# Performance work log

Measured on AMD Instinct MI355X. Metric: run time of the kernel, lower is better.

The kernel has to match this reference:

```python
import jax, jax.numpy as jnp
import numpy as np

N = 100000   # nodes
E = 3200000  # edges
F = 128      # num_features
H = 20       # hidden dim (hard-coded in source)
C = 10       # num_classes
EPS = 1e-5


def setup_inputs() -> dict:
    key = jax.random.key(0)
    ks = jax.random.split(key, 16)
    x = jax.random.normal(ks[0], (N, F), jnp.float32)
    edge_index = jax.random.randint(ks[1], (2, E), 0, N)
    edge_weights = jnp.ones((E,), jnp.float32)

    def lin_init(k, fan_in, shape):
        s = 1.0 / np.sqrt(fan_in)
        return jax.random.uniform(k, shape, jnp.float32, -s, s)

    return {
        "x": x,
        "edge_index": edge_index,
        "edge_weights": edge_weights,
        "W1": lin_init(ks[2], F, (F, H)), "b1": jnp.zeros((H,), jnp.float32),
        "g1": jnp.ones((H,), jnp.float32), "be1": jnp.zeros((H,), jnp.float32),
        "W2": lin_init(ks[3], H, (H, H)), "b2": jnp.zeros((H,), jnp.float32),
        "g2": jnp.ones((H,), jnp.float32), "be2": jnp.zeros((H,), jnp.float32),
        "W3": lin_init(ks[4], H, (H, H)), "b3": jnp.zeros((H,), jnp.float32),
        "Wl": lin_init(ks[5], 3 * H, (3 * H, C)), "bl": lin_init(ks[6], 3 * H, (C,)),
    }


def gcn_conv(x, src, dst, ew, W, b, n):
    # PyG GCNConv: transform, add self-loops, symmetric deg^-1/2 normalization, scatter-add.
    h = x @ W  # [N, out]
    loop = jnp.arange(n)
    src2 = jnp.concatenate([src, loop])
    dst2 = jnp.concatenate([dst, loop])
    ew2 = jnp.concatenate([ew, jnp.ones((n,), x.dtype)])
    deg = jax.ops.segment_sum(ew2, dst2, num_segments=n)
    dinv = jnp.where(deg > 0, jax.lax.rsqrt(deg), 0.0)
    coef = (dinv[src2] * ew2 * dinv[dst2])[:, None]  # [E+N, 1]
    out = jax.ops.segment_sum(h[src2] * coef, dst2, num_segments=n)
    return out + b


def batch_norm(x, g, b):
    m = x.mean(axis=0)
    v = x.var(axis=0)
    return (x - m) * jax.lax.rsqrt(v + EPS) * g + b


def reference(x, edge_index, edge_weights, W1, b1, g1, be1, W2, b2, g2, be2, W3, b3, Wl, bl):
    src, dst = edge_index[0], edge_index[1]
    n = x.shape[0]
    o1 = batch_norm(jax.nn.relu(gcn_conv(x, src, dst, edge_weights, W1, b1, n)), g1, be1)
    o2 = batch_norm(jax.nn.relu(gcn_conv(o1, src, dst, edge_weights, W2, b2, n)), g2, be2)
    o3 = jax.nn.relu(gcn_conv(o2, src, dst, edge_weights, W3, b3, n))
    emb = jnp.concatenate([o1, o2, o3], axis=1)  # [N, 60]
    return emb @ Wl + bl
```

## Files before the change

kernel.cpp:

```cpp
#include <hip/hip_runtime.h>
#include <hip/hip_fp16.h>


#define HD 20
#define HSS 32
#define EPS 1e-5f
#define BSH 7
#define NBMAX 1024
#define CAP 5632
#define CAPE 2816

typedef float __attribute__((ext_vector_type(4))) f4v;

__device__ __forceinline__ float4 ntld4(const float* p) {
    f4v v = __builtin_nontemporal_load((const f4v*)p);
    return make_float4(v.x, v.y, v.z, v.w);
}

__global__ __launch_bounds__(1024)
void init_kernel(int* bcnt, float* stats, float* zero20, int nbv) {
    int t = threadIdx.x;
    if (t < nbv) bcnt[t] = 0;
    if (t < 80) stats[t] = 0.0f;
    if (t < HD) zero20[t] = 0.0f;
}

__global__ __launch_bounds__(256)
void bucket_hist_kernel(const int* __restrict__ dst, int* __restrict__ bcnt,
                        int E, int chunk, int nbv) {
    __shared__ int lh[NBMAX];
    for (int i = threadIdx.x; i < nbv; i += 256) lh[i] = 0;
    __syncthreads();
    int s = blockIdx.x * chunk;
    int e = s + chunk; if (e > E) e = E;
    for (int j = s + threadIdx.x; j < e; j += 256)
        atomicAdd(&lh[dst[j] >> BSH], 1);
    __syncthreads();
    for (int i = threadIdx.x; i < nbv; i += 256)
        if (lh[i]) atomicAdd(&bcnt[i], lh[i]);
}

__global__ __launch_bounds__(1024)
void bucket_scan_kernel(const int* __restrict__ bcnt, int* __restrict__ bstart,
                        int* __restrict__ bcur, int* __restrict__ row_start,
                        int n, int E, int nbv) {
    __shared__ int s[1024];
    int t = threadIdx.x;
    int v = (t < nbv) ? bcnt[t] : 0;
    s[t] = v;
    __syncthreads();
    for (int off = 1; off < 1024; off <<= 1) {
        int u = (t >= off) ? s[t - off] : 0;
        __syncthreads();
        s[t] += u;
        __syncthreads();
    }
    if (t < nbv) { int st = s[t] - v; bstart[t] = st; bcur[t] = st; }
    if (t == 0) { bstart[nbv] = E; row_start[n] = E; }
}

__global__ __launch_bounds__(256)
void scatter_kernel(const int* __restrict__ src, const int* __restrict__ dst,
                    const float* __restrict__ ew, int* __restrict__ bcur,
                    int2* __restrict__ tmp, int E, int chunk, int nbv) {
    __shared__ int lh[NBMAX];
    __shared__ int lbase[NBMAX];
    for (int i = threadIdx.x; i < nbv; i += 256) lh[i] = 0;
    __syncthreads();
    int s = blockIdx.x * chunk;
    int e = s + chunk; if (e > E) e = E;
    for (int j = s + threadIdx.x; j < e; j += 256)
        atomicAdd(&lh[dst[j] >> BSH], 1);
    __syncthreads();
    for (int i = threadIdx.x; i < nbv; i += 256) {
        int c = lh[i];
        lbase[i] = c ? atomicAdd(&bcur[i], c) : 0;
        lh[i] = 0;
    }
    __syncthreads();
    for (int j = s + threadIdx.x; j < e; j += 256) {
        int d = dst[j];
        int b = d >> BSH;
        int pos = atomicAdd(&lh[b], 1);
        tmp[lbase[b] + pos] = make_int2(src[j] | ((d & ((1 << BSH) - 1)) << 20),
                                        __float_as_int(ew[j]));
    }
}

__global__ __launch_bounds__(256)
void finalize_kernel(const int2* __restrict__ tmp, const int* __restrict__ bstart,
                     int2* __restrict__ se, int* __restrict__ row_start,
                     float* __restrict__ dinv, int n) {
    __shared__ int hist[128];
    __shared__ float degs[128];
    __shared__ int off[128];
    __shared__ int cur[128];
    __shared__ int2 stage[CAP];
    int b = blockIdx.x;
    int s0 = bstart[b], s1 = bstart[b + 1];
    int cnt = s1 - s0;
    int t = threadIdx.x;
    if (t < 128) { hist[t] = 0; degs[t] = 0.0f; cur[t] = 0; }
    __syncthreads();
    for (int j = s0 + t; j < s1; j += 256) {
        int2 r = tmp[j];
        int l = r.x >> 20;
        atomicAdd(&hist[l], 1);
        atomicAdd(&degs[l], __int_as_float(r.y));
    }
    __syncthreads();
    if (t < 128) off[t] = hist[t];
    __syncthreads();
    for (int o = 1; o < 128; o <<= 1) {
        int u = (t < 128 && t >= o) ? off[t - o] : 0;
        __syncthreads();
        if (t < 128) off[t] += u;
        __syncthreads();
    }
    if (t < 128) {
        int node = (b << BSH) + t;
        if (node < n) {
            row_start[node] = s0 + off[t] - hist[t];
            dinv[node] = rsqrtf(1.0f + degs[t]);
        }
    }
    __syncthreads();
    if (cnt <= CAP) {
        for (int j = s0 + t; j < s1; j += 256) {
            int2 r = tmp[j];
            int l = r.x >> 20;
            int p = (off[l] - hist[l]) + atomicAdd(&cur[l], 1);
            stage[p] = make_int2(r.x & 0xFFFFF, r.y);
        }
        __syncthreads();
        for (int k = t; k < cnt; k += 256) se[s0 + k] = stage[k];
    } else {
        for (int j = s0 + t; j < s1; j += 256) {
            int2 r = tmp[j];
            int l = r.x >> 20;
            int p = (off[l] - hist[l]) + atomicAdd(&cur[l], 1);
            se[s0 + p] = make_int2(r.x & 0xFFFFF, r.y);
        }
    }
}

template<int FIN, int NPB>
__global__ __launch_bounds__(256)
void gemm_kernel(const float* __restrict__ in, const float* __restrict__ W,
                 const float* __restrict__ cvec, const float* __restrict__ dinv,
                 __half* __restrict__ hs, int n) {
    __shared__ float sWt[HD][FIN + 4];
    __shared__ float sIn[NPB][FIN + 4];
    __shared__ float sC[HD];
    for (int i = threadIdx.x; i < FIN * HD; i += 256) {
        int k = i / HD, f = i % HD;
        sWt[f][k] = W[i];
    }
    if (threadIdx.x < HD) sC[threadIdx.x] = cvec[threadIdx.x];
    int base = blockIdx.x * NPB;
    int nb = n - base; if (nb > NPB) nb = NPB;
    int lim = n * FIN;
    const int Q = FIN / 4;
    for (int i = threadIdx.x; i < NPB * Q; i += 256) {
        int row = i / Q, c = (i % Q) * 4;
        int g = (base + row) * FIN + c;
        *(float4*)&sIn[row][c] = (g < lim) ? ntld4(&in[g])
                                           : make_float4(0.f, 0.f, 0.f, 0.f);
    }
    __syncthreads();
    for (int idx = threadIdx.x; idx < NPB * HD; idx += 256) {
        int nl = idx / HD, f = idx % HD;
        float4 a = make_float4(0.f, 0.f, 0.f, 0.f);
        #pragma unroll 4
        for (int k = 0; k < FIN; k += 4) {
            float4 x4 = *(const float4*)&sIn[nl][k];
            float4 w4 = *(const float4*)&sWt[f][k];
            a.x = fmaf(x4.x, w4.x, a.x);
            a.y = fmaf(x4.y, w4.y, a.y);
            a.z = fmaf(x4.z, w4.z, a.z);
            a.w = fmaf(x4.w, w4.w, a.w);
        }
        if (nl < nb)
            hs[(size_t)(base + nl) * HSS + f] = __float2half_rn(
                (((a.x + a.y) + (a.z + a.w)) + sC[f]) * dinv[base + nl]);
    }
}

#define FMA4(A, V, W) \
    A.x = fmaf(V.x, W, A.x); A.y = fmaf(V.y, W, A.y); \
    A.z = fmaf(V.z, W, A.z); A.w = fmaf(V.w, W, A.w);

__device__ __forceinline__ float4 h4f2(uint2 u) {
    float2 f0 = __half22float2(*reinterpret_cast<const __half2*>(&u.x));
    float2 f1 = __half22float2(*reinterpret_cast<const __half2*>(&u.y));
    return make_float4(f0.x, f0.y, f1.x, f1.y);
}

#define ROWLD(Q0, Q1, Q2, SRC) { \
    const uint4* pa_ = (const uint4*)(hsb + (size_t)(SRC) * HSS); \
    Q0 = pa_[0]; Q1 = pa_[1]; \
    Q2 = *(const uint2*)(pa_ + 2); }

#define AGG_LOOP(EDGEAT)                                                     \
    {                                                                        \
        int2 e = EDGEAT(j);                                                  \
        float w = __int_as_float(e.y);                                       \
        uint4 c0, c1; uint2 c2; ROWLD(c0, c1, c2, e.x)                       \
        while (true) {                                                       \
            int jn = j + 4;                                                  \
            bool more = jn < s1;                                             \
            int jp = more ? jn : j;             \
            int2 en = EDGEAT(jp);                                            \
            uint4 n0, n1; uint2 n2; ROWLD(n0, n1, n2, en.x)                  \
            float wn = __int_as_float(en.y);                                 \
            float4 v0 = h4f2(make_uint2(c0.x, c0.y));                        \
            float4 v1 = h4f2(make_uint2(c0.z, c0.w));                        \
            float4 v2 = h4f2(make_uint2(c1.x, c1.y));                        \
            float4 v3 = h4f2(make_uint2(c1.z, c1.w));                        \
            float4 v4 = h4f2(c2);                                            \
            FMA4(a0, v0, w) FMA4(a1, v1, w) FMA4(a2, v2, w)                  \
            FMA4(a3, v3, w) FMA4(a4, v4, w)                                  \
            if (!more) break;                                                \
            j = jn; w = wn;                                                  \
            c0 = n0; c1 = n1; c2 = n2;                                       \
        }                                                                    \
    }

#define EDGE_LDS(jj) sse[(jj) - sb0]
#define EDGE_GBL(jj) se[(jj)]

template<int MODE>
__global__ __launch_bounds__(256)
void agg_kernel(const __half* __restrict__ hsb, const float* __restrict__ dinv,
                const int* __restrict__ row_start, const int2* __restrict__ se,
                const float* __restrict__ bias, float* __restrict__ out,
                float* __restrict__ stat_sum, float* __restrict__ stat_sq,
                const float* __restrict__ o1, const float* __restrict__ o2,
                const float* __restrict__ Wlp, const float* __restrict__ blp,
                int n) {
    __shared__ int2 sse[CAPE];
    __shared__ float ls[HD], lq[HD];
    __shared__ float sW[600];
    __shared__ float sb[10];
    int base = blockIdx.x * 64;
    int nEnd = base + 64; if (nEnd > n) nEnd = n;
    int sb0 = row_start[base];
    int sb1 = row_start[nEnd];
    int span = sb1 - sb0;
    bool ok = (span <= CAPE);
    if (MODE == 0) {
        if (threadIdx.x < HD) { ls[threadIdx.x] = 0.0f; lq[threadIdx.x] = 0.0f; }
    } else {
        for (int i = threadIdx.x; i < 600; i += 256) sW[i] = Wlp[i];
        if (threadIdx.x < 10) sb[threadIdx.x] = blp[threadIdx.x];
    }
    if (ok) {
        for (int k = threadIdx.x; k < span; k += 256) {
            long long v = __builtin_nontemporal_load(
                (const long long*)(se + sb0 + k));
            sse[k] = *(const int2*)&v;
        }
    }
    __syncthreads();
    int i = base + (threadIdx.x >> 2), lane = threadIdx.x & 3;
    if (i < n) {
        float di = dinv[i];
        int s0 = row_start[i], s1 = row_start[i + 1];
        float4 a0, a1, a2, a3, a4;
        if (lane == 0) {
            uint4 y0, y1; uint2 y2;
            ROWLD(y0, y1, y2, i)
            a0 = h4f2(make_uint2(y0.x, y0.y));
            a1 = h4f2(make_uint2(y0.z, y0.w));
            a2 = h4f2(make_uint2(y1.x, y1.y));
            a3 = h4f2(make_uint2(y1.z, y1.w));
            a4 = h4f2(y2);
        } else {
            a0 = a1 = a2 = a3 = a4 = make_float4(0.f, 0.f, 0.f, 0.f);
        }
        int j = s0 + lane;
        if (j < s1) {
            if (ok) { AGG_LOOP(EDGE_LDS) }
            else    { AGG_LOOP(EDGE_GBL) }
        }
        #define REDX(A, M) \
            A.x += __shfl_xor(A.x, M); A.y += __shfl_xor(A.y, M); \
            A.z += __shfl_xor(A.z, M); A.w += __shfl_xor(A.w, M);
        #define RED4L(A) REDX(A, 1) REDX(A, 2)
        RED4L(a0) RED4L(a1) RED4L(a2) RED4L(a3) RED4L(a4)
        float4 acc[5] = {a0, a1, a2, a3, a4};
        float va[HD];
        #pragma unroll
        for (int q = 0; q < 5; ++q) {
            float4 bb = *(const float4*)(bias + 4 * q);
            va[4 * q + 0] = fmaxf(fmaf(acc[q].x, di, bb.x), 0.0f);
            va[4 * q + 1] = fmaxf(fmaf(acc[q].y, di, bb.y), 0.0f);
            va[4 * q + 2] = fmaxf(fmaf(acc[q].z, di, bb.z), 0.0f);
            va[4 * q + 3] = fmaxf(fmaf(acc[q].w, di, bb.w), 0.0f);
        }
        if (MODE == 0) {
            if (lane == 0) {
                #pragma unroll
                for (int q = 0; q < 5; ++q) {
                    ((float4*)out)[i * 5 + q] = make_float4(
                        va[4 * q], va[4 * q + 1], va[4 * q + 2], va[4 * q + 3]);
                    int f = 4 * q;
                    atomicAdd(&ls[f + 0], va[f + 0]); atomicAdd(&lq[f + 0], va[f + 0] * va[f + 0]);
                    atomicAdd(&ls[f + 1], va[f + 1]); atomicAdd(&lq[f + 1], va[f + 1] * va[f + 1]);
                    atomicAdd(&ls[f + 2], va[f + 2]); atomicAdd(&lq[f + 2], va[f + 2] * va[f + 2]);
                    atomicAdd(&ls[f + 3], va[f + 3]); atomicAdd(&lq[f + 3], va[f + 3] * va[f + 3]);
                }
            }
        } else {
            float r1[HD], r2[HD];
            #pragma unroll
            for (int q = 0; q < 5; ++q) {
                *(float4*)&r1[4 * q] = ((const float4*)(o1 + (size_t)i * HD))[q];
                *(float4*)&r2[4 * q] = ((const float4*)(o2 + (size_t)i * HD))[q];
            }
            for (int c = lane; c < 10; c += 4) {
                float s = sb[c];
                #pragma unroll
                for (int k = 0; k < HD; ++k) s = fmaf(r1[k], sW[k * 10 + c], s);
                #pragma unroll
                for (int k = 0; k < HD; ++k) s = fmaf(r2[k], sW[(HD + k) * 10 + c], s);
                #pragma unroll
                for (int k = 0; k < HD; ++k) s = fmaf(va[k], sW[(2 * HD + k) * 10 + c], s);
                out[(size_t)i * 10 + c] = s;
            }
        }
    }
    if (MODE == 0) {
        __syncthreads();
        if (threadIdx.x < HD) {
            atomicAdd(&stat_sum[threadIdx.x], ls[threadIdx.x]);
            atomicAdd(&stat_sq[threadIdx.x], lq[threadIdx.x]);
        }
    }
}

__global__ __launch_bounds__(512)
void bn_adjust_kernel(const float* __restrict__ sum, const float* __restrict__ sq,
                      const float* __restrict__ g, const float* __restrict__ be,
                      const float* __restrict__ W, float* __restrict__ scsh_out,
                      float* __restrict__ Wp, float* __restrict__ cvec, int n) {
    __shared__ float ssc[HD], ssh[HD];
    int t = threadIdx.x;
    if (t < HD) {
        float inv_n = 1.0f / (float)n;
        float m = sum[t] * inv_n;
        float var = sq[t] * inv_n - m * m;
        float sc = g[t] * rsqrtf(var + EPS);
        float sh = be[t] - m * sc;
        ssc[t] = sc; ssh[t] = sh;
        scsh_out[t] = sc; scsh_out[HD + t] = sh;
    }
    __syncthreads();
    if (t < HD * HD) Wp[t] = ssc[t / HD] * W[t];
    if (t < HD) {
        float acc = 0.0f;
        #pragma unroll
        for (int k = 0; k < HD; ++k) acc = fmaf(ssh[k], W[k * HD + t], acc);
        cvec[t] = acc;
    }
}

__global__ __launch_bounds__(640)
void bn_adjust2_kernel(const float* __restrict__ sum, const float* __restrict__ sq,
                       const float* __restrict__ g, const float* __restrict__ be,
                       const float* __restrict__ W, float* __restrict__ scsh_out,
                       float* __restrict__ Wp, float* __restrict__ cvec,
                       const float* __restrict__ Wl, const float* __restrict__ bl,
                       const float* __restrict__ scsh1,
                       float* __restrict__ Wlp, float* __restrict__ blp, int n) {
    __shared__ float ssc[HD], ssh[HD];
    int t = threadIdx.x;
    if (t < HD) {
        float inv_n = 1.0f / (float)n;
        float m = sum[t] * inv_n;
        float var = sq[t] * inv_n - m * m;
        float sc = g[t] * rsqrtf(var + EPS);
        float sh = be[t] - m * sc;
        ssc[t] = sc; ssh[t] = sh;
        scsh_out[t] = sc; scsh_out[HD + t] = sh;
    }
    __syncthreads();
    if (t < HD * HD) Wp[t] = ssc[t / HD] * W[t];
    if (t < HD) {
        float acc = 0.0f;
        #pragma unroll
        for (int k = 0; k < HD; ++k) acc = fmaf(ssh[k], W[k * HD + t], acc);
        cvec[t] = acc;
    }
    if (t < 600) {
        int k = t / 10;
        float s = (k < HD) ? scsh1[k] : (k < 2 * HD) ? ssc[k - HD] : 1.0f;
        Wlp[t] = s * Wl[t];
    }
    if (t < 10) {
        float acc = bl[t];
        #pragma unroll
        for (int k = 0; k < HD; ++k) acc = fmaf(scsh1[HD + k], Wl[k * 10 + t], acc);
        #pragma unroll
        for (int k = 0; k < HD; ++k) acc = fmaf(ssh[k], Wl[(HD + k) * 10 + t], acc);
        blp[t] = acc;
    }
}

extern "C" void kernel_launch(void* const* d_in, const int* in_sizes, int n_in,
                              void* d_out, int out_size, void* d_ws, size_t ws_size,
                              hipStream_t stream) {
    const float* x   = (const float*)d_in[0];
    const int*   ei  = (const int*)d_in[1];
    const float* ew  = (const float*)d_in[2];
    const float* W1  = (const float*)d_in[3];
    const float* b1  = (const float*)d_in[4];
    const float* g1  = (const float*)d_in[5];
    const float* be1 = (const float*)d_in[6];
    const float* W2  = (const float*)d_in[7];
    const float* b2  = (const float*)d_in[8];
    const float* g2  = (const float*)d_in[9];
    const float* be2 = (const float*)d_in[10];
    const float* W3  = (const float*)d_in[11];
    const float* b3  = (const float*)d_in[12];
    const float* Wl  = (const float*)d_in[13];
    const float* bl  = (const float*)d_in[14];
    float* out = (float*)d_out;

    const int F = in_sizes[3] / HD;
    const int N = in_sizes[0] / F;
    const int E = in_sizes[2];
    const int* src = ei;
    const int* dst = ei + E;
    const int nbv = (N + 127) >> BSH;

    char* p = (char*)d_ws;
    auto alloc = [&](size_t bytes) -> void* {
        void* r = (void*)p;
        p += (bytes + 255) & ~(size_t)255;
        return r;
    };
    size_t nh4 = (size_t)N * HD * 4;
    int2*  se      = (int2*) alloc((size_t)E * 8);
    char*  regionA = (char*) alloc((size_t)E * 8);
    float* o2r     = (float*)alloc(nh4);
    float* dinv    = (float*)alloc((size_t)N * 4);
    int*   row_start = (int*)alloc((size_t)(N + 1) * 4);
    int*   bcnt    = (int*)  alloc(NBMAX * 4);
    int*   bstart  = (int*)  alloc((NBMAX + 1) * 4);
    int*   bcur    = (int*)  alloc(NBMAX * 4);
    float* stats   = (float*)alloc(80 * 4);
    float* scsh    = (float*)alloc(80 * 4);
    float* zero20  = (float*)alloc(20 * 4);
    float* W2p     = (float*)alloc(400 * 4);
    float* c2      = (float*)alloc(20 * 4);
    float* W3p     = (float*)alloc(400 * 4);
    float* c3      = (float*)alloc(20 * 4);
    float* Wlp     = (float*)alloc(600 * 4);
    float* blp     = (float*)alloc(12 * 4);

    int2*   tmp = (int2*)regionA;
    __half* hs  = (__half*)regionA;
    float*  o1r = (float*)(regionA + 2 * nh4);

    const int B = 256;
    const int GB = 512;
    const int chunk = (E + GB - 1) / GB;
    int gAgg = (4 * N + B - 1) / B;

    hipLaunchKernelGGL(init_kernel, dim3(1), dim3(1024), 0, stream, bcnt, stats, zero20, nbv);
    hipLaunchKernelGGL(bucket_hist_kernel, dim3(GB), dim3(B), 0, stream, dst, bcnt, E, chunk, nbv);
    hipLaunchKernelGGL(bucket_scan_kernel, dim3(1), dim3(1024), 0, stream,
                       bcnt, bstart, bcur, row_start, N, E, nbv);
    hipLaunchKernelGGL(scatter_kernel, dim3(GB), dim3(B), 0, stream,
                       src, dst, ew, bcur, tmp, E, chunk, nbv);
    hipLaunchKernelGGL(finalize_kernel, dim3(nbv), dim3(B), 0, stream,
                       tmp, bstart, se, row_start, dinv, N);

    hipLaunchKernelGGL((gemm_kernel<128, 16>), dim3((N + 15) / 16), dim3(B), 0, stream,
                       x, W1, zero20, dinv, hs, N);
    hipLaunchKernelGGL((agg_kernel<0>), dim3(gAgg), dim3(B), 0, stream,
                       hs, dinv, row_start, se, b1, o1r,
                       stats, stats + 20, nullptr, nullptr, nullptr, nullptr, N);
    hipLaunchKernelGGL(bn_adjust_kernel, dim3(1), dim3(512), 0, stream,
                       stats, stats + 20, g1, be1, W2, scsh, W2p, c2, N);

    hipLaunchKernelGGL((gemm_kernel<HD, 64>), dim3((N + 63) / 64), dim3(B), 0, stream,
                       o1r, W2p, c2, dinv, hs, N);
    hipLaunchKernelGGL((agg_kernel<0>), dim3(gAgg), dim3(B), 0, stream,
                       hs, dinv, row_start, se, b2, o2r,
                       stats + 40, stats + 60, nullptr, nullptr, nullptr, nullptr, N);
    hipLaunchKernelGGL(bn_adjust2_kernel, dim3(1), dim3(640), 0, stream,
                       stats + 40, stats + 60, g2, be2, W3, scsh + 40, W3p, c3,
                       Wl, bl, scsh, Wlp, blp, N);

    hipLaunchKernelGGL((gemm_kernel<HD, 64>), dim3((N + 63) / 64), dim3(B), 0, stream,
                       o2r, W3p, c3, dinv, hs, N);
    hipLaunchKernelGGL((agg_kernel<1>), dim3(gAgg), dim3(B), 0, stream,
                       hs, dinv, row_start, se, b3, out,
                       nullptr, nullptr, o1r, o2r, Wlp, blp, N);
}
```

Before: 523.2 us.

## Add all-ones edge-weight fast path with compact edge list and dense rows

Checks on the device whether every edge weight equals one. If so, the scatter, finalize and aggregation kernels use a 4-byte source-only edge list instead of 8-byte (src, weight) pairs, compute degree from counts, and drop the per-edge multiply. This halves edge-list traffic and doubles the LDS staging capacity. Separately, the fp16 hidden rows are stored at a 20-element (40-byte) stride instead of a padded 32-element stride, which cuts gather bytes but leaves rows not aligned to 16 bytes. The fallback path for general weights is kept, and the check adds a read of ew in the histogram pass.

```diff
diff --git a/kernel.cpp b/kernel.cpp
--- a/kernel.cpp
+++ b/kernel.cpp
@@ -3,7 +3,6 @@
 
 
 #define HD 20
-#define HSS 32
 #define EPS 1e-5f
 #define BSH 7
 #define NBMAX 1024
@@ -18,26 +17,33 @@
 }
 
 __global__ __launch_bounds__(1024)
-void init_kernel(int* bcnt, float* stats, float* zero20, int nbv) {
+void init_kernel(int* bcnt, float* stats, float* zero20, int* eflag, int nbv) {
     int t = threadIdx.x;
     if (t < nbv) bcnt[t] = 0;
     if (t < 80) stats[t] = 0.0f;
     if (t < HD) zero20[t] = 0.0f;
+    if (t == 0) eflag[0] = 1;
 }
 
 __global__ __launch_bounds__(256)
-void bucket_hist_kernel(const int* __restrict__ dst, int* __restrict__ bcnt,
+void bucket_hist_kernel(const int* __restrict__ dst, const float* __restrict__ ew,
+                        int* __restrict__ bcnt, int* __restrict__ eflag,
                         int E, int chunk, int nbv) {
     __shared__ int lh[NBMAX];
+    __shared__ int okf;
+    if (threadIdx.x == 0) okf = 1;
     for (int i = threadIdx.x; i < nbv; i += 256) lh[i] = 0;
     __syncthreads();
     int s = blockIdx.x * chunk;
     int e = s + chunk; if (e > E) e = E;
-    for (int j = s + threadIdx.x; j < e; j += 256)
+    for (int j = s + threadIdx.x; j < e; j += 256) {
         atomicAdd(&lh[dst[j] >> BSH], 1);
+        if (ew[j] != 1.0f) okf = 0;
+    }
     __syncthreads();
     for (int i = threadIdx.x; i < nbv; i += 256)
         if (lh[i]) atomicAdd(&bcnt[i], lh[i]);
+    if (threadIdx.x == 0 && !okf) eflag[0] = 0;
 }
 
 __global__ __launch_bounds__(1024)
@@ -61,8 +67,9 @@
 
 __global__ __launch_bounds__(256)
 void scatter_kernel(const int* __restrict__ src, const int* __restrict__ dst,
-                    const float* __restrict__ ew, int* __restrict__ bcur,
-                    int2* __restrict__ tmp, int E, int chunk, int nbv) {
+                    const float* __restrict__ ew, const int* __restrict__ eflag,
+                    int* __restrict__ bcur, int2* __restrict__ tmp,
+                    int E, int chunk, int nbv) {
     __shared__ int lh[NBMAX];
     __shared__ int lbase[NBMAX];
     for (int i = threadIdx.x; i < nbv; i += 256) lh[i] = 0;
@@ -78,17 +85,28 @@
         lh[i] = 0;
     }
     __syncthreads();
-    for (int j = s + threadIdx.x; j < e; j += 256) {
-        int d = dst[j];
-        int b = d >> BSH;
-        int pos = atomicAdd(&lh[b], 1);
-        tmp[lbase[b] + pos] = make_int2(src[j] | ((d & ((1 << BSH) - 1)) << 20),
-                                        __float_as_int(ew[j]));
+    if (eflag[0]) {
+        int* tmp4 = (int*)tmp;
+        for (int j = s + threadIdx.x; j < e; j += 256) {
+            int d = dst[j];
+            int b = d >> BSH;
+            int pos = atomicAdd(&lh[b], 1);
+            tmp4[lbase[b] + pos] = src[j] | ((d & ((1 << BSH) - 1)) << 20);
+        }
+    } else {
+        for (int j = s + threadIdx.x; j < e; j += 256) {
+            int d = dst[j];
+            int b = d >> BSH;
+            int pos = atomicAdd(&lh[b], 1);
+            tmp[lbase[b] + pos] = make_int2(src[j] | ((d & ((1 << BSH) - 1)) << 20),
+                                           __float_as_int(ew[j]));
+        }
     }
 }
 
 __global__ __launch_bounds__(256)
 void finalize_kernel(const int2* __restrict__ tmp, const int* __restrict__ bstart,
+                     const int* __restrict__ eflag,
                      int2* __restrict__ se, int* __restrict__ row_start,
                      float* __restrict__ dinv, int n) {
     __shared__ int hist[128];
@@ -96,17 +114,26 @@
     __shared__ int off[128];
     __shared__ int cur[128];
     __shared__ int2 stage[CAP];
+    int* stage4 = (int*)stage;
+    const int* tmp4 = (const int*)tmp;
+    int* se4 = (int*)se;
+    bool f4 = eflag[0] != 0;
     int b = blockIdx.x;
     int s0 = bstart[b], s1 = bstart[b + 1];
     int cnt = s1 - s0;
     int t = threadIdx.x;
     if (t < 128) { hist[t] = 0; degs[t] = 0.0f; cur[t] = 0; }
     __syncthreads();
-    for (int j = s0 + t; j < s1; j += 256) {
-        int2 r = tmp[j];
-        int l = r.x >> 20;
-        atomicAdd(&hist[l], 1);
-        atomicAdd(&degs[l], __int_as_float(r.y));
+    if (f4) {
+        for (int j = s0 + t; j < s1; j += 256)
+            atomicAdd(&hist[tmp4[j] >> 20], 1);
+    } else {
+        for (int j = s0 + t; j < s1; j += 256) {
+            int2 r = tmp[j];
+            int l = r.x >> 20;
+            atomicAdd(&hist[l], 1);
+            atomicAdd(&degs[l], __int_as_float(r.y));
+        }
     }
     __syncthreads();
     if (t < 128) off[t] = hist[t];
@@ -121,25 +148,46 @@
         int node = (b << BSH) + t;
         if (node < n) {
             row_start[node] = s0 + off[t] - hist[t];
-            dinv[node] = rsqrtf(1.0f + degs[t]);
-        }
-    }
-    __syncthreads();
-    if (cnt <= CAP) {
-        for (int j = s0 + t; j < s1; j += 256) {
-            int2 r = tmp[j];
-            int l = r.x >> 20;
-            int p = (off[l] - hist[l]) + atomicAdd(&cur[l], 1);
-            stage[p] = make_int2(r.x & 0xFFFFF, r.y);
-        }
-        __syncthreads();
-        for (int k = t; k < cnt; k += 256) se[s0 + k] = stage[k];
+            float dg = f4 ? (float)hist[t] : degs[t];
+            dinv[node] = rsqrtf(1.0f + dg);
+        }
+    }
+    __syncthreads();
+    if (f4) {
+        if (cnt <= 2 * CAP) {
+            for (int j = s0 + t; j < s1; j += 256) {
+                int r = tmp4[j];
+                int l = r >> 20;
+                int p = (off[l] - hist[l]) + atomicAdd(&cur[l], 1);
+                stage4[p] = r & 0xFFFFF;
+            }
+            __syncthreads();
+            for (int k = t; k < cnt; k += 256) se4[s0 + k] = stage4[k];
+        } else {
+            for (int j = s0 + t; j < s1; j += 256) {
+                int r = tmp4[j];
+                int l = r >> 20;
+                int p = (off[l] - hist[l]) + atomicAdd(&cur[l], 1);
+                se4[s0 + p] = r & 0xFFFFF;
+            }
+        }
     } else {
-        for (int j = s0 + t; j < s1; j += 256) {
-            int2 r = tmp[j];
-            int l = r.x >> 20;
-            int p = (off[l] - hist[l]) + atomicAdd(&cur[l], 1);
-            se[s0 + p] = make_int2(r.x & 0xFFFFF, r.y);
+        if (cnt <= CAP) {
+            for (int j = s0 + t; j < s1; j += 256) {
+                int2 r = tmp[j];
+                int l = r.x >> 20;
+                int p = (off[l] - hist[l]) + atomicAdd(&cur[l], 1);
+                stage[p] = make_int2(r.x & 0xFFFFF, r.y);
+            }
+            __syncthreads();
+            for (int k = t; k < cnt; k += 256) se[s0 + k] = stage[k];
+        } else {
+            for (int j = s0 + t; j < s1; j += 256) {
+                int2 r = tmp[j];
+                int l = r.x >> 20;
+                int p = (off[l] - hist[l]) + atomicAdd(&cur[l], 1);
+                se[s0 + p] = make_int2(r.x & 0xFFFFF, r.y);
+            }
         }
     }
 }
@@ -181,7 +229,7 @@
             a.w = fmaf(x4.w, w4.w, a.w);
         }
         if (nl < nb)
-            hs[(size_t)(base + nl) * HSS + f] = __float2half_rn(
+            hs[(size_t)(base + nl) * HD + f] = __float2half_rn(
                 (((a.x + a.y) + (a.z + a.w)) + sC[f]) * dinv[base + nl]);
     }
 }
@@ -189,6 +237,9 @@
 #define FMA4(A, V, W) \
     A.x = fmaf(V.x, W, A.x); A.y = fmaf(V.y, W, A.y); \
     A.z = fmaf(V.z, W, A.z); A.w = fmaf(V.w, W, A.w);
+
+#define ADD4(A, V) \
+    A.x += V.x; A.y += V.y; A.z += V.z; A.w += V.w;
 
 __device__ __forceinline__ float4 h4f2(uint2 u) {
     float2 f0 = __half22float2(*reinterpret_cast<const __half2*>(&u.x));
@@ -197,9 +248,10 @@
 }
 
 #define ROWLD(Q0, Q1, Q2, SRC) { \
-    const uint4* pa_ = (const uint4*)(hsb + (size_t)(SRC) * HSS); \
-    Q0 = pa_[0]; Q1 = pa_[1]; \
-    Q2 = *(const uint2*)(pa_ + 2); }
+    const char* rp_ = (const char*)hsb + (size_t)(SRC) * 40; \
+    Q0 = *(const uint4*)rp_; \
+    Q1 = *(const uint4*)(rp_ + 16); \
+    Q2 = *(const uint2*)(rp_ + 32); }
 
 #define AGG_LOOP(EDGEAT)                                                     \
     {                                                                        \
@@ -209,7 +261,7 @@
         while (true) {                                                       \
             int jn = j + 4;                                                  \
             bool more = jn < s1;                                             \
-            int jp = more ? jn : j;             \
+            int jp = more ? jn : j;                                          \
             int2 en = EDGEAT(jp);                                            \
             uint4 n0, n1; uint2 n2; ROWLD(n0, n1, n2, en.x)                  \
             float wn = __int_as_float(en.y);                                 \
@@ -226,28 +278,57 @@
         }                                                                    \
     }
 
-#define EDGE_LDS(jj) sse[(jj) - sb0]
-#define EDGE_GBL(jj) se[(jj)]
+#define AGG_LOOP4(EDGEAT)                                                    \
+    {                                                                        \
+        int e = EDGEAT(j);                                                   \
+        uint4 c0, c1; uint2 c2; ROWLD(c0, c1, c2, e)                         \
+        while (true) {                                                       \
+            int jn = j + 4;                                                  \
+            bool more = jn < s1;                                             \
+            int jp = more ? jn : j;                                          \
+            int en = EDGEAT(jp);                                             \
+            uint4 n0, n1; uint2 n2; ROWLD(n0, n1, n2, en)                    \
+            float4 v0 = h4f2(make_uint2(c0.x, c0.y));                        \
+            float4 v1 = h4f2(make_uint2(c0.z, c0.w));                        \
+            float4 v2 = h4f2(make_uint2(c1.x, c1.y));                        \
+            float4 v3 = h4f2(make_uint2(c1.z, c1.w));                        \
+            float4 v4 = h4f2(c2);                                            \
+            ADD4(a0, v0) ADD4(a1, v1) ADD4(a2, v2)                           \
+            ADD4(a3, v3) ADD4(a4, v4)                                        \
+            if (!more) break;                                                \
+            j = jn;                                                          \
+            c0 = n0; c1 = n1; c2 = n2;                                       \
+        }                                                                    \
+    }
+
+#define EDGE_LDS(jj)  sse[(jj) - sb0]
+#define EDGE_GBL(jj)  se[(jj)]
+#define EDGE_LDS4(jj) sse4[(jj) - sb0]
+#define EDGE_GBL4(jj) se4[(jj)]
 
 template<int MODE>
 __global__ __launch_bounds__(256)
 void agg_kernel(const __half* __restrict__ hsb, const float* __restrict__ dinv,
                 const int* __restrict__ row_start, const int2* __restrict__ se,
+                const int* __restrict__ eflag,
                 const float* __restrict__ bias, float* __restrict__ out,
                 float* __restrict__ stat_sum, float* __restrict__ stat_sq,
                 const float* __restrict__ o1, const float* __restrict__ o2,
                 const float* __restrict__ Wlp, const float* __restrict__ blp,
                 int n) {
     __shared__ int2 sse[CAPE];
+    int* sse4 = (int*)sse;
+    const int* se4 = (const int*)se;
     __shared__ float ls[HD], lq[HD];
     __shared__ float sW[600];
     __shared__ float sb[10];
+    bool f4 = eflag[0] != 0;
     int base = blockIdx.x * 64;
     int nEnd = base + 64; if (nEnd > n) nEnd = n;
     int sb0 = row_start[base];
     int sb1 = row_start[nEnd];
     int span = sb1 - sb0;
-    bool ok = (span <= CAPE);
+    bool ok = span <= (f4 ? 2 * CAPE : CAPE);
     if (MODE == 0) {
         if (threadIdx.x < HD) { ls[threadIdx.x] = 0.0f; lq[threadIdx.x] = 0.0f; }
     } else {
@@ -255,10 +336,15 @@
         if (threadIdx.x < 10) sb[threadIdx.x] = blp[threadIdx.x];
     }
     if (ok) {
-        for (int k = threadIdx.x; k < span; k += 256) {
-            long long v = __builtin_nontemporal_load(
-                (const long long*)(se + sb0 + k));
-            sse[k] = *(const int2*)&v;
+        if (f4) {
+            for (int k = threadIdx.x; k < span; k += 256)
+                sse4[k] = __builtin_nontemporal_load(se4 + sb0 + k);
+        } else {
+            for (int k = threadIdx.x; k < span; k += 256) {
+                long long v = __builtin_nontemporal_load(
+                    (const long long*)(se + sb0 + k));
+                sse[k] = *(const int2*)&v;
+            }
         }
     }
     __syncthreads();
@@ -280,8 +366,13 @@
         }
         int j = s0 + lane;
         if (j < s1) {
-            if (ok) { AGG_LOOP(EDGE_LDS) }
-            else    { AGG_LOOP(EDGE_GBL) }
+            if (f4) {
+                if (ok) { AGG_LOOP4(EDGE_LDS4) }
+                else    { AGG_LOOP4(EDGE_GBL4) }
+            } else {
+                if (ok) { AGG_LOOP(EDGE_LDS) }
+                else    { AGG_LOOP(EDGE_GBL) }
+            }
         }
         #define REDX(A, M) \
             A.x += __shfl_xor(A.x, M); A.y += __shfl_xor(A.y, M); \
@@ -458,6 +549,7 @@
     float* c3      = (float*)alloc(20 * 4);
     float* Wlp     = (float*)alloc(600 * 4);
     float* blp     = (float*)alloc(12 * 4);
+    int*   eflag   = (int*)  alloc(4);
 
     int2*   tmp = (int2*)regionA;
     __half* hs  = (__half*)regionA;
@@ -468,19 +560,21 @@
     const int chunk = (E + GB - 1) / GB;
     int gAgg = (4 * N + B - 1) / B;
 
-    hipLaunchKernelGGL(init_kernel, dim3(1), dim3(1024), 0, stream, bcnt, stats, zero20, nbv);
-    hipLaunchKernelGGL(bucket_hist_kernel, dim3(GB), dim3(B), 0, stream, dst, bcnt, E, chunk, nbv);
+    hipLaunchKernelGGL(init_kernel, dim3(1), dim3(1024), 0, stream,
+                       bcnt, stats, zero20, eflag, nbv);
+    hipLaunchKernelGGL(bucket_hist_kernel, dim3(GB), dim3(B), 0, stream,
+                       dst, ew, bcnt, eflag, E, chunk, nbv);
     hipLaunchKernelGGL(bucket_scan_kernel, dim3(1), dim3(1024), 0, stream,
                        bcnt, bstart, bcur, row_start, N, E, nbv);
     hipLaunchKernelGGL(scatter_kernel, dim3(GB), dim3(B), 0, stream,
-                       src, dst, ew, bcur, tmp, E, chunk, nbv);
+                       src, dst, ew, eflag, bcur, tmp, E, chunk, nbv);
     hipLaunchKernelGGL(finalize_kernel, dim3(nbv), dim3(B), 0, stream,
-                       tmp, bstart, se, row_start, dinv, N);
+                       tmp, bstart, eflag, se, row_start, dinv, N);
 
     hipLaunchKernelGGL((gemm_kernel<128, 16>), dim3((N + 15) / 16), dim3(B), 0, stream,
                        x, W1, zero20, dinv, hs, N);
     hipLaunchKernelGGL((agg_kernel<0>), dim3(gAgg), dim3(B), 0, stream,
-                       hs, dinv, row_start, se, b1, o1r,
+                       hs, dinv, row_start, se, eflag, b1, o1r,
                        stats, stats + 20, nullptr, nullptr, nullptr, nullptr, N);
     hipLaunchKernelGGL(bn_adjust_kernel, dim3(1), dim3(512), 0, stream,
                        stats, stats + 20, g1, be1, W2, scsh, W2p, c2, N);
@@ -488,7 +582,7 @@
     hipLaunchKernelGGL((gemm_kernel<HD, 64>), dim3((N + 63) / 64), dim3(B), 0, stream,
                        o1r, W2p, c2, dinv, hs, N);
     hipLaunchKernelGGL((agg_kernel<0>), dim3(gAgg), dim3(B), 0, stream,
-                       hs, dinv, row_start, se, b2, o2r,
+                       hs, dinv, row_start, se, eflag, b2, o2r,
                        stats + 40, stats + 60, nullptr, nullptr, nullptr, nullptr, N);
     hipLaunchKernelGGL(bn_adjust2_kernel, dim3(1), dim3(640), 0, stream,
                        stats + 40, stats + 60, g2, be2, W3, scsh + 40, W3p, c3,
@@ -497,6 +591,6 @@
     hipLaunchKernelGGL((gemm_kernel<HD, 64>), dim3((N + 63) / 64), dim3(B), 0, stream,
                        o2r, W3p, c3, dinv, hs, N);
     hipLaunchKernelGGL((agg_kernel<1>), dim3(gAgg), dim3(B), 0, stream,
-                       hs, dinv, row_start, se, b3, out,
+                       hs, dinv, row_start, se, eflag, b3, out,
                        nullptr, nullptr, o1r, o2r, Wlp, blp, N);
 }
```

New measurement: 492.7 us. 5.8% less time.
